# Kernel tuning notes

Measured on AMD Instinct MI355X. Metric: run time of the kernel, lower is better.

Reference implementation:

```python
import jax, jax.numpy as jnp
import numpy as np

B, T, D_MODEL, H, HD = 2, 2048, 2048, 16, 128
TOTAL = H * HD


def setup_inputs() -> dict:
    key = jax.random.key(0)
    ks = jax.random.split(key, 7)
    s = 1.0 / np.sqrt(D_MODEL)
    x = jax.random.normal(ks[0], (B, T, D_MODEL), dtype=jnp.float32)
    cos = jax.random.uniform(ks[1], (T, HD), dtype=jnp.float32)
    sin = jax.random.uniform(ks[2], (T, HD), dtype=jnp.float32)
    Wq = jax.random.normal(ks[3], (D_MODEL, TOTAL), dtype=jnp.float32) * s
    Wk = jax.random.normal(ks[4], (D_MODEL, TOTAL), dtype=jnp.float32) * s
    Wv = jax.random.normal(ks[5], (D_MODEL, TOTAL), dtype=jnp.float32) * s
    Wo = jax.random.normal(ks[6], (TOTAL, D_MODEL), dtype=jnp.float32) * s
    return {"x": x, "cos": cos, "sin": sin, "Wq": Wq, "Wk": Wk, "Wv": Wv, "Wo": Wo}


def rotate_half(x):
    x1, x2 = jnp.split(x, 2, axis=-1)
    return jnp.concatenate([-x2, x1], axis=-1)


def reference(x, cos, sin, Wq, Wk, Wv, Wo):
    b, t, _ = x.shape
    # QKV projections -> [B, H, T, HD]
    q = (x @ Wq).reshape(b, t, H, HD).transpose(0, 2, 1, 3)
    k = (x @ Wk).reshape(b, t, H, HD).transpose(0, 2, 1, 3)
    v = (x @ Wv).reshape(b, t, H, HD).transpose(0, 2, 1, 3)
    # RoPE (cos/sin broadcast [T,HD] -> [B,H,T,HD])
    q = q * cos + rotate_half(q) * sin
    k = k * cos + rotate_half(k) * sin
    # causal SDPA (kv_cache=None branch), eval mode -> no dropout
    scale = HD ** -0.5
    scores = jnp.einsum('bhqd,bhkd->bhqk', q, k) * scale
    causal = jnp.tril(jnp.ones((t, t), dtype=bool))
    scores = jnp.where(causal, scores, jnp.asarray(-1e9, scores.dtype))
    attn = jax.nn.softmax(scores, axis=-1)
    out = jnp.einsum('bhqk,bhkd->bhqd', attn, v)
    out = out.transpose(0, 2, 1, 3).reshape(b, t, TOTAL)
    return out @ Wo, k, v
```

## Files before the change

kernel.cpp:

```cpp
#include <hip/hip_runtime.h>


typedef __bf16 bf16;
typedef __attribute__((ext_vector_type(8))) __bf16 bf16x8;
typedef __attribute__((ext_vector_type(4))) __bf16 bf16x4;
typedef __attribute__((ext_vector_type(4))) float f32x4;

__device__ __forceinline__ void gload_lds16(const void* g, void* l) {
  __builtin_amdgcn_global_load_lds((const __attribute__((address_space(1))) void*)g,
                                   (__attribute__((address_space(3))) void*)l, 16, 0, 0);
}

__global__ __launch_bounds__(256) void k_convert(const float* __restrict__ in,
                                                 bf16* __restrict__ out, int n4) {
  int i = blockIdx.x * 256 + threadIdx.x;
  if (i >= n4) return;
  float4 v = ((const float4*)in)[i];
  bf16x4 o;
  o.x = (bf16)v.x; o.y = (bf16)v.y; o.z = (bf16)v.z; o.w = (bf16)v.w;
  ((bf16x4*)out)[i] = o;
}

__global__ __launch_bounds__(256) void k_transpose_w(
    const float* __restrict__ W0, const float* __restrict__ W1,
    const float* __restrict__ W2, const float* __restrict__ W3,
    bf16* __restrict__ T0, bf16* __restrict__ T1,
    bf16* __restrict__ T2, bf16* __restrict__ T3) {
  __shared__ float tile[32][33];
  const float* W; bf16* To;
  switch (blockIdx.z) {
    case 0: W = W0; To = T0; break;
    case 1: W = W1; To = T1; break;
    case 2: W = W2; To = T2; break;
    default: W = W3; To = T3; break;
  }
  int n0 = blockIdx.x * 32, k0 = blockIdx.y * 32;
  int tx = threadIdx.x, ty = threadIdx.y;
#pragma unroll
  for (int j = 0; j < 4; ++j)
    tile[ty + 8 * j][tx] = W[(size_t)(k0 + ty + 8 * j) * 2048 + n0 + tx];
  __syncthreads();
#pragma unroll
  for (int j = 0; j < 4; ++j)
    To[(size_t)(n0 + ty + 8 * j) * 2048 + k0 + tx] = (bf16)tile[tx][ty + 8 * j];
}

template <int MODE>
__global__ __launch_bounds__(256) void k_gemm(
    const bf16* __restrict__ A, const bf16* __restrict__ B0,
    const bf16* __restrict__ B1, const bf16* __restrict__ B2,
    bf16* __restrict__ o0, bf16* __restrict__ o1, bf16* __restrict__ o2,
    float* __restrict__ outf) {
  __shared__ __align__(16) bf16 Al[128 * 64];
  __shared__ __align__(16) bf16 Bl[128 * 64];
  const bf16* Bt; bf16* outb = nullptr;
  if (MODE == 0) {
    switch (blockIdx.z) {
      case 0: Bt = B0; outb = o0; break;
      case 1: Bt = B1; outb = o1; break;
      default: Bt = B2; outb = o2; break;
    }
  } else {
    Bt = B0;
  }
  int t = threadIdx.x;
  int wv = t >> 6, lane = t & 63, lr = lane & 15, lg = lane >> 4;
  int wr = wv >> 1, wc = wv & 1;
  int row0 = blockIdx.x * 128, col0 = blockIdx.y * 128;
  f32x4 acc[4][4] = {};
  for (int kt = 0; kt < 32; ++kt) {
    int k0 = kt * 64;
#pragma unroll
    for (int it = 0; it < 4; ++it) {
      int ci = it * 256 + t;
      int r = ci >> 3, c8 = (ci & 7) * 8;
      int base = __builtin_amdgcn_readfirstlane(it * 256 + (t & ~63));
      gload_lds16(A + (size_t)(row0 + r) * 2048 + k0 + c8, Al + (size_t)base * 8);
      gload_lds16(Bt + (size_t)(col0 + r) * 2048 + k0 + c8, Bl + (size_t)base * 8);
    }
    __syncthreads();
#pragma unroll
    for (int kk = 0; kk < 2; ++kk) {
      bf16x8 af[4], bfr[4];
#pragma unroll
      for (int mf = 0; mf < 4; ++mf)
        af[mf] = *(const bf16x8*)(Al + (wr * 64 + mf * 16 + lr) * 64 + kk * 32 + lg * 8);
#pragma unroll
      for (int nf = 0; nf < 4; ++nf)
        bfr[nf] = *(const bf16x8*)(Bl + (wc * 64 + nf * 16 + lr) * 64 + kk * 32 + lg * 8);
#pragma unroll
      for (int mf = 0; mf < 4; ++mf)
#pragma unroll
        for (int nf = 0; nf < 4; ++nf)
          acc[mf][nf] = __builtin_amdgcn_mfma_f32_16x16x32_bf16(af[mf], bfr[nf], acc[mf][nf], 0, 0, 0);
    }
    __syncthreads();
  }
#pragma unroll
  for (int mf = 0; mf < 4; ++mf)
#pragma unroll
    for (int nf = 0; nf < 4; ++nf)
#pragma unroll
      for (int r = 0; r < 4; ++r) {
        int row = row0 + wr * 64 + mf * 16 + lg * 4 + r;
        int col = col0 + wc * 64 + nf * 16 + lr;
        float v = acc[mf][nf][r];
        if (MODE == 0) {
          int b = row >> 11, tt = row & 2047, h = col >> 7, d = col & 127;
          outb[(size_t)((b * 16 + h) * 2048 + tt) * 128 + d] = (bf16)v;
        } else {
          outf[(size_t)row * 2048 + col] = v;
        }
      }
}

__global__ __launch_bounds__(256) void k_rope(
    bf16* __restrict__ q, bf16* __restrict__ k, const bf16* __restrict__ v,
    const float* __restrict__ cosb, const float* __restrict__ sinb,
    float* __restrict__ kout, float* __restrict__ vout) {
  int tid = blockIdx.x * 256 + threadIdx.x;
  int d = tid & 63;
  int row = tid >> 6;
  int t = row & 2047;
  size_t base = (size_t)row * 128;
  float c1 = cosb[t * 128 + d], c2 = cosb[t * 128 + 64 + d];
  float s1 = sinb[t * 128 + d], s2 = sinb[t * 128 + 64 + d];
  float qlo = (float)q[base + d], qhi = (float)q[base + 64 + d];
  float klo = (float)k[base + d], khi = (float)k[base + 64 + d];
  float ql = qlo * c1 - qhi * s1, qh = qhi * c2 + qlo * s2;
  float kl = klo * c1 - khi * s1, kh = khi * c2 + klo * s2;
  q[base + d] = (bf16)ql; q[base + 64 + d] = (bf16)qh;
  k[base + d] = (bf16)kl; k[base + 64 + d] = (bf16)kh;
  kout[base + d] = kl; kout[base + 64 + d] = kh;
  vout[base + d] = (float)v[base + d];
  vout[base + 64 + d] = (float)v[base + 64 + d];
}

__global__ __launch_bounds__(256) void k_vt(const bf16* __restrict__ v,
                                            bf16* __restrict__ vt) {
  __shared__ bf16 tile[32][33];
  int bh = blockIdx.z;
  int t0 = blockIdx.x * 32, d0 = blockIdx.y * 32;
  int tx = threadIdx.x, ty = threadIdx.y;
  const bf16* vb = v + (size_t)bh * 2048 * 128;
  bf16* vtb = vt + (size_t)bh * 128 * 2048;
#pragma unroll
  for (int j = 0; j < 4; ++j)
    tile[ty + 8 * j][tx] = vb[(size_t)(t0 + ty + 8 * j) * 128 + d0 + tx];
  __syncthreads();
#pragma unroll
  for (int j = 0; j < 4; ++j)
    vtb[(size_t)(d0 + ty + 8 * j) * 2048 + t0 + tx] = tile[tx][ty + 8 * j];
}

__global__ __launch_bounds__(256, 2) void k_attn(
    const bf16* __restrict__ Q, const bf16* __restrict__ Kr,
    const bf16* __restrict__ Vt, bf16* __restrict__ O) {
  __shared__ __align__(16) bf16 Pl[4][2][16][64];
  int t = threadIdx.x, wv = t >> 6, lane = t & 63, lr = lane & 15, lg = lane >> 4;
  int qb = (int)gridDim.x - 1 - (int)blockIdx.x;
  int bh = blockIdx.y;
  int qbase = qb * 128;
  const bf16* Qb = Q + (size_t)bh * 2048 * 128;
  const bf16* Kb = Kr + (size_t)bh * 2048 * 128;
  const bf16* Vb = Vt + (size_t)bh * 128 * 2048;
  int wq[2] = {qbase + wv * 16, qbase + 64 + wv * 16};
  bf16x8 qf[2][4];
#pragma unroll
  for (int mf = 0; mf < 2; ++mf)
#pragma unroll
    for (int df = 0; df < 4; ++df)
      qf[mf][df] = *(const bf16x8*)(Qb + (size_t)(wq[mf] + lr) * 128 + df * 32 + lg * 8);
  f32x4 od[2][8] = {};
  float m_run[2][4], l_run[2][4];
#pragma unroll
  for (int mf = 0; mf < 2; ++mf)
#pragma unroll
    for (int r = 0; r < 4; ++r) { m_run[mf][r] = -1e30f; l_run[mf][r] = 0.f; }
  const float scale = 0.08838834764831845f;
  int nkt = 2 * qb + 2;
  for (int kt = 0; kt < nkt; ++kt) {
    int kv0 = kt * 64;
    f32x4 s[2][4] = {};
#pragma unroll
    for (int c = 0; c < 4; ++c) {
      bf16x8 kf[4];
#pragma unroll
      for (int df = 0; df < 4; ++df)
        kf[df] = *(const bf16x8*)(Kb + (size_t)(kv0 + c * 16 + lr) * 128 + df * 32 + lg * 8);
#pragma unroll
      for (int mf = 0; mf < 2; ++mf)
#pragma unroll
        for (int df = 0; df < 4; ++df)
          s[mf][c] = __builtin_amdgcn_mfma_f32_16x16x32_bf16(qf[mf][df], kf[df], s[mf][c], 0, 0, 0);
    }
    bool act0 = (kv0 <= wq[0] + 15);
#pragma unroll
    for (int mf = 0; mf < 2; ++mf) {
      if (mf == 0 && !act0) continue;
      float corr[4];
#pragma unroll
      for (int r = 0; r < 4; ++r) {
        int qrow = wq[mf] + lg * 4 + r;
        float sv[4];
#pragma unroll
        for (int c = 0; c < 4; ++c) {
          sv[c] = s[mf][c][r] * scale;
          if (kv0 + c * 16 + lr > qrow) sv[c] = -1e30f;
        }
        float mx = fmaxf(fmaxf(sv[0], sv[1]), fmaxf(sv[2], sv[3]));
        mx = fmaxf(mx, __shfl_xor(mx, 1));
        mx = fmaxf(mx, __shfl_xor(mx, 2));
        mx = fmaxf(mx, __shfl_xor(mx, 4));
        mx = fmaxf(mx, __shfl_xor(mx, 8));
        float mnew = fmaxf(m_run[mf][r], mx);
        float cr = __expf(m_run[mf][r] - mnew);
        float pv0 = __expf(sv[0] - mnew), pv1 = __expf(sv[1] - mnew);
        float pv2 = __expf(sv[2] - mnew), pv3 = __expf(sv[3] - mnew);
        float rs = pv0 + pv1 + pv2 + pv3;
        rs += __shfl_xor(rs, 1); rs += __shfl_xor(rs, 2);
        rs += __shfl_xor(rs, 4); rs += __shfl_xor(rs, 8);
        l_run[mf][r] = l_run[mf][r] * cr + rs;
        m_run[mf][r] = mnew;
        corr[r] = cr;
        int row = lg * 4 + r, sw = (row & 7) * 8;
        Pl[wv][mf][row][(0 * 16 + lr) ^ sw] = (bf16)pv0;
        Pl[wv][mf][row][(1 * 16 + lr) ^ sw] = (bf16)pv1;
        Pl[wv][mf][row][(2 * 16 + lr) ^ sw] = (bf16)pv2;
        Pl[wv][mf][row][(3 * 16 + lr) ^ sw] = (bf16)pv3;
      }
#pragma unroll
      for (int db = 0; db < 8; ++db)
#pragma unroll
        for (int r = 0; r < 4; ++r) od[mf][db][r] *= corr[r];
    }
    __builtin_amdgcn_sched_barrier(0);
    __builtin_amdgcn_s_waitcnt(0xc07f);
    __builtin_amdgcn_sched_barrier(0);
    bf16x8 pa[2][2];
#pragma unroll
    for (int mf = 0; mf < 2; ++mf) {
      if (mf == 0 && !act0) continue;
#pragma unroll
      for (int kk = 0; kk < 2; ++kk)
        pa[mf][kk] = *(const bf16x8*)(&Pl[wv][mf][lr][(kk * 32 + lg * 8) ^ ((lr & 7) * 8)]);
    }
#pragma unroll
    for (int kk = 0; kk < 2; ++kk)
#pragma unroll
      for (int db = 0; db < 8; ++db) {
        bf16x8 vf = *(const bf16x8*)(Vb + (size_t)(db * 16 + lr) * 2048 + kv0 + kk * 32 + lg * 8);
        if (act0)
          od[0][db] = __builtin_amdgcn_mfma_f32_16x16x32_bf16(pa[0][kk], vf, od[0][db], 0, 0, 0);
        od[1][db] = __builtin_amdgcn_mfma_f32_16x16x32_bf16(pa[1][kk], vf, od[1][db], 0, 0, 0);
      }
  }
  int b = bh >> 4, h = bh & 15;
#pragma unroll
  for (int mf = 0; mf < 2; ++mf)
#pragma unroll
    for (int db = 0; db < 8; ++db)
#pragma unroll
      for (int r = 0; r < 4; ++r) {
        int q = wq[mf] + lg * 4 + r;
        float v = od[mf][db][r] / l_run[mf][r];
        O[(size_t)(b * 2048 + q) * 2048 + h * 128 + db * 16 + lr] = (bf16)v;
      }
}

extern "C" void kernel_launch(void* const* d_in, const int* in_sizes, int n_in,
                              void* d_out, int out_size, void* d_ws, size_t ws_size,
                              hipStream_t stream) {
  const float* x    = (const float*)d_in[0];
  const float* cosb = (const float*)d_in[1];
  const float* sinb = (const float*)d_in[2];
  const float* Wq   = (const float*)d_in[3];
  const float* Wk   = (const float*)d_in[4];
  const float* Wv   = (const float*)d_in[5];
  const float* Wo   = (const float*)d_in[6];
  float* out  = (float*)d_out;
  float* kout = out + (size_t)8388608;
  float* vout = out + (size_t)16777216;

  char* ws = (char*)d_ws;
  bf16* xb  = (bf16*)(ws);
  bf16* WqT = (bf16*)(ws + (size_t)16777216);
  bf16* WkT = (bf16*)(ws + (size_t)25165824);
  bf16* WvT = (bf16*)(ws + (size_t)33554432);
  bf16* WoT = (bf16*)(ws + (size_t)41943040);
  bf16* qb  = (bf16*)(ws + (size_t)50331648);
  bf16* kb  = (bf16*)(ws + (size_t)67108864);
  bf16* vb  = (bf16*)(ws + (size_t)83886080);
  bf16* vt  = (bf16*)(ws + (size_t)100663296);
  bf16* ao  = xb;

  k_convert<<<8192, 256, 0, stream>>>(x, xb, 2097152);
  k_transpose_w<<<dim3(64, 64, 4), dim3(32, 8), 0, stream>>>(Wq, Wk, Wv, Wo,
                                                             WqT, WkT, WvT, WoT);
  k_gemm<0><<<dim3(32, 16, 3), 256, 0, stream>>>(xb, WqT, WkT, WvT,
                                                 qb, kb, vb, nullptr);
  k_rope<<<16384, 256, 0, stream>>>(qb, kb, vb, cosb, sinb, kout, vout);
  k_vt<<<dim3(64, 4, 32), dim3(32, 8), 0, stream>>>(vb, vt);
  k_attn<<<dim3(16, 32), 256, 0, stream>>>(qb, kb, vt, ao);
  k_gemm<1><<<dim3(32, 16, 1), 256, 0, stream>>>(ao, WoT, nullptr, nullptr,
                                                 nullptr, nullptr, nullptr, out);
}
```

Measured before the change: 674.5 us.

## Compute transposed S^T in attention and move P into MFMA operands via shuffles instead of LDS

```diff
diff --git a/kernel.cpp b/kernel.cpp
--- a/kernel.cpp
+++ b/kernel.cpp
@@ -156,7 +156,6 @@
 __global__ __launch_bounds__(256, 2) void k_attn(
     const bf16* __restrict__ Q, const bf16* __restrict__ Kr,
     const bf16* __restrict__ Vt, bf16* __restrict__ O) {
-  __shared__ __align__(16) bf16 Pl[4][2][16][64];
   int t = threadIdx.x, wv = t >> 6, lane = t & 63, lr = lane & 15, lg = lane >> 4;
   int qb = (int)gridDim.x - 1 - (int)blockIdx.x;
   int bh = blockIdx.y;
@@ -172,13 +171,11 @@
     for (int df = 0; df < 4; ++df)
       qf[mf][df] = *(const bf16x8*)(Qb + (size_t)(wq[mf] + lr) * 128 + df * 32 + lg * 8);
   f32x4 od[2][8] = {};
-  float m_run[2][4], l_run[2][4];
-#pragma unroll
-  for (int mf = 0; mf < 2; ++mf)
-#pragma unroll
-    for (int r = 0; r < 4; ++r) { m_run[mf][r] = -1e30f; l_run[mf][r] = 0.f; }
+  float m_run[2] = {-1e30f, -1e30f}, l_run[2] = {0.f, 0.f};
   const float scale = 0.08838834764831845f;
   int nkt = 2 * qb + 2;
+  int s0l = lr + 32 * (lg & 1), s1l = lr + 32 * (lg & 1) + 16;
+  bool hi = (lg >> 1) != 0;
   for (int kt = 0; kt < nkt; ++kt) {
     int kv0 = kt * 64;
     f32x4 s[2][4] = {};
@@ -192,80 +189,103 @@
       for (int mf = 0; mf < 2; ++mf)
 #pragma unroll
         for (int df = 0; df < 4; ++df)
-          s[mf][c] = __builtin_amdgcn_mfma_f32_16x16x32_bf16(qf[mf][df], kf[df], s[mf][c], 0, 0, 0);
-    }
+          s[mf][c] = __builtin_amdgcn_mfma_f32_16x16x32_bf16(kf[df], qf[mf][df], s[mf][c], 0, 0, 0);
+    }
+    bf16x8 vf[2][8];
+#pragma unroll
+    for (int kk = 0; kk < 2; ++kk)
+#pragma unroll
+      for (int db = 0; db < 8; ++db)
+        vf[kk][db] = *(const bf16x8*)(Vb + (size_t)(db * 16 + lr) * 2048 + kv0 + kk * 32 + lg * 8);
     bool act0 = (kv0 <= wq[0] + 15);
 #pragma unroll
     for (int mf = 0; mf < 2; ++mf) {
       if (mf == 0 && !act0) continue;
+      int q = wq[mf] + lr;
+      float p[4][4];
+#pragma unroll
+      for (int c = 0; c < 4; ++c)
+#pragma unroll
+        for (int r = 0; r < 4; ++r) {
+          float v = s[mf][c][r] * scale;
+          p[c][r] = (kv0 + c * 16 + lg * 4 + r > q) ? -1e30f : v;
+        }
+      float mx = -1e30f;
+#pragma unroll
+      for (int c = 0; c < 4; ++c)
+#pragma unroll
+        for (int r = 0; r < 4; ++r) mx = fmaxf(mx, p[c][r]);
+      mx = fmaxf(mx, __shfl_xor(mx, 16));
+      mx = fmaxf(mx, __shfl_xor(mx, 32));
+      float mnew = fmaxf(m_run[mf], mx);
+      float cr = __expf(m_run[mf] - mnew);
+      float rs = 0.f;
+#pragma unroll
+      for (int c = 0; c < 4; ++c)
+#pragma unroll
+        for (int r = 0; r < 4; ++r) {
+          p[c][r] = __expf(p[c][r] - mnew);
+          rs += p[c][r];
+        }
+      rs += __shfl_xor(rs, 16);
+      rs += __shfl_xor(rs, 32);
+      l_run[mf] = l_run[mf] * cr + rs;
+      m_run[mf] = mnew;
       float corr[4];
 #pragma unroll
-      for (int r = 0; r < 4; ++r) {
-        int qrow = wq[mf] + lg * 4 + r;
-        float sv[4];
-#pragma unroll
-        for (int c = 0; c < 4; ++c) {
-          sv[c] = s[mf][c][r] * scale;
-          if (kv0 + c * 16 + lr > qrow) sv[c] = -1e30f;
+      for (int r = 0; r < 4; ++r)
+        corr[r] = __shfl(cr, (lane & 48) | (lg * 4 + r));
+#pragma unroll
+      for (int db = 0; db < 8; ++db)
+#pragma unroll
+        for (int r = 0; r < 4; ++r) od[mf][db][r] *= corr[r];
+      unsigned pk[4][2];
+#pragma unroll
+      for (int c = 0; c < 4; ++c)
+#pragma unroll
+        for (int h = 0; h < 2; ++h) {
+          bf16 b0 = (bf16)p[c][2 * h], b1 = (bf16)p[c][2 * h + 1];
+          unsigned u0 = *(const unsigned short*)&b0;
+          unsigned u1 = *(const unsigned short*)&b1;
+          pk[c][h] = (u1 << 16) | u0;
         }
-        float mx = fmaxf(fmaxf(sv[0], sv[1]), fmaxf(sv[2], sv[3]));
-        mx = fmaxf(mx, __shfl_xor(mx, 1));
-        mx = fmaxf(mx, __shfl_xor(mx, 2));
-        mx = fmaxf(mx, __shfl_xor(mx, 4));
-        mx = fmaxf(mx, __shfl_xor(mx, 8));
-        float mnew = fmaxf(m_run[mf][r], mx);
-        float cr = __expf(m_run[mf][r] - mnew);
-        float pv0 = __expf(sv[0] - mnew), pv1 = __expf(sv[1] - mnew);
-        float pv2 = __expf(sv[2] - mnew), pv3 = __expf(sv[3] - mnew);
-        float rs = pv0 + pv1 + pv2 + pv3;
-        rs += __shfl_xor(rs, 1); rs += __shfl_xor(rs, 2);
-        rs += __shfl_xor(rs, 4); rs += __shfl_xor(rs, 8);
-        l_run[mf][r] = l_run[mf][r] * cr + rs;
-        m_run[mf][r] = mnew;
-        corr[r] = cr;
-        int row = lg * 4 + r, sw = (row & 7) * 8;
-        Pl[wv][mf][row][(0 * 16 + lr) ^ sw] = (bf16)pv0;
-        Pl[wv][mf][row][(1 * 16 + lr) ^ sw] = (bf16)pv1;
-        Pl[wv][mf][row][(2 * 16 + lr) ^ sw] = (bf16)pv2;
-        Pl[wv][mf][row][(3 * 16 + lr) ^ sw] = (bf16)pv3;
+#pragma unroll
+      for (int kk = 0; kk < 2; ++kk) {
+        unsigned a0 = __shfl(pk[2 * kk][0], s0l);
+        unsigned a1 = __shfl(pk[2 * kk][1], s0l);
+        unsigned a2 = __shfl(pk[2 * kk][0], s1l);
+        unsigned a3 = __shfl(pk[2 * kk][1], s1l);
+        unsigned b0 = __shfl(pk[2 * kk + 1][0], s0l);
+        unsigned b1 = __shfl(pk[2 * kk + 1][1], s0l);
+        unsigned b2 = __shfl(pk[2 * kk + 1][0], s1l);
+        unsigned b3 = __shfl(pk[2 * kk + 1][1], s1l);
+        union { unsigned u[4]; bf16x8 v; } pw;
+        pw.u[0] = hi ? b0 : a0;
+        pw.u[1] = hi ? b1 : a1;
+        pw.u[2] = hi ? b2 : a2;
+        pw.u[3] = hi ? b3 : a3;
+#pragma unroll
+        for (int db = 0; db < 8; ++db)
+          od[mf][db] = __builtin_amdgcn_mfma_f32_16x16x32_bf16(pw.v, vf[kk][db], od[mf][db], 0, 0, 0);
       }
-#pragma unroll
-      for (int db = 0; db < 8; ++db)
-#pragma unroll
-        for (int r = 0; r < 4; ++r) od[mf][db][r] *= corr[r];
-    }
-    __builtin_amdgcn_sched_barrier(0);
-    __builtin_amdgcn_s_waitcnt(0xc07f);
-    __builtin_amdgcn_sched_barrier(0);
-    bf16x8 pa[2][2];
-#pragma unroll
-    for (int mf = 0; mf < 2; ++mf) {
-      if (mf == 0 && !act0) continue;
-#pragma unroll
-      for (int kk = 0; kk < 2; ++kk)
-        pa[mf][kk] = *(const bf16x8*)(&Pl[wv][mf][lr][(kk * 32 + lg * 8) ^ ((lr & 7) * 8)]);
-    }
-#pragma unroll
-    for (int kk = 0; kk < 2; ++kk)
-#pragma unroll
-      for (int db = 0; db < 8; ++db) {
-        bf16x8 vf = *(const bf16x8*)(Vb + (size_t)(db * 16 + lr) * 2048 + kv0 + kk * 32 + lg * 8);
-        if (act0)
-          od[0][db] = __builtin_amdgcn_mfma_f32_16x16x32_bf16(pa[0][kk], vf, od[0][db], 0, 0, 0);
-        od[1][db] = __builtin_amdgcn_mfma_f32_16x16x32_bf16(pa[1][kk], vf, od[1][db], 0, 0, 0);
-      }
+    }
   }
   int b = bh >> 4, h = bh & 15;
 #pragma unroll
-  for (int mf = 0; mf < 2; ++mf)
+  for (int mf = 0; mf < 2; ++mf) {
+    float ld[4];
+#pragma unroll
+    for (int r = 0; r < 4; ++r)
+      ld[r] = __shfl(l_run[mf], (lane & 48) | (lg * 4 + r));
 #pragma unroll
     for (int db = 0; db < 8; ++db)
 #pragma unroll
       for (int r = 0; r < 4; ++r) {
         int q = wq[mf] + lg * 4 + r;
-        float v = od[mf][db][r] / l_run[mf][r];
+        float v = od[mf][db][r] / ld[r];
         O[(size_t)(b * 2048 + q) * 2048 + h * 128 + db * 16 + lr] = (bf16)v;
       }
+  }
 }
 
 extern "C" void kernel_launch(void* const* d_in, const int* in_sizes, int n_in,
```

After: 605.2 us. -10.3%, faster.
